# Performance work log

Hardware: AMD Instinct MI355X
Metric: run time of the kernel (lower is better)

Reference implementation:

```python
import jax, jax.numpy as jnp
import numpy as np

K = 9            # connections per output pixel
GA = 2           # global additional samples
RA = 2           # relative additional samples
VS = 4 + GA + RA # 2^rank neighbours + sampled
REGION = 12      # int(0.25 * 48) per spatial dim
MMULT = 0.1
MIN_SIGMA = 0.05
SIGMA_SCALE = 0.05
SIGMA_BOOST = 2.0


def setup_inputs() -> dict:
    key = jax.random.key(0)
    ks = jax.random.split(key, 8)
    b, cin, h, w = 8, 128, 48, 48
    cout = 256
    hidden = cin * 4

    def lin_init(k, fan_out, fan_in):
        bound = 1.0 / np.sqrt(fan_in)
        kw, kb = jax.random.split(k)
        W = jax.random.uniform(kw, (fan_out, fan_in), minval=-bound, maxval=bound, dtype=jnp.float32)
        bb = jax.random.uniform(kb, (fan_out,), minval=-bound, maxval=bound, dtype=jnp.float32)
        return W, bb

    x = jax.random.normal(ks[0], (b, cin, h, w), dtype=jnp.float32)
    W1, b1 = lin_init(ks[1], hidden, 2)          # toparams layer 1 (adaptive=False -> 2 coord inputs)
    W2, b2 = lin_init(ks[2], 3 * K, hidden)      # toparams layer 2 -> k means (2d) + k sigmas
    Wu, bu = lin_init(ks[3], cout, K * cin)      # unify linear
    gints = jax.random.randint(ks[4], (b, h, w, K, GA, 2), 0, h, dtype=jnp.int32)      # global samples (h==w)
    roff = jax.random.randint(ks[5], (b, h, w, K, RA, 2), 0, REGION, dtype=jnp.int32)  # relative offsets
    return {"x": x, "W1": W1, "b1": b1, "W2": W2, "b2": b2, "Wu": Wu, "bu": bu,
            "gints": gints, "roff": roff}


def reference(x, W1, b1, W2, b2, Wu, bu, gints, roff):
    b, c, h, w = x.shape
    s = jnp.array([h, w], dtype=x.dtype)                       # spatial range per dim
    s_int = jnp.array([h, w], dtype=jnp.int32)

    # normalized coordinate grid in [0,1], (h, w, 2) with [.,.,0]=row, [.,.,1]=col
    rows = jnp.arange(h, dtype=x.dtype) / (h - 1)
    cols = jnp.arange(w, dtype=x.dtype) / (w - 1)
    coords = jnp.stack(jnp.meshgrid(rows, cols, indexing='ij'), axis=-1)

    # hypernetwork: per-pixel coords -> K 2d mean offsets + K sigmas
    inp = jnp.broadcast_to(coords, (b, h, w, 2))
    hid = jax.nn.relu(inp @ W1.T + b1)
    params = hid @ W2.T + b2                                   # (b,h,w,3K)
    means_raw = params[..., :2 * K].reshape(b, h, w, K, 2)
    sig_raw = params[..., 2 * K:]                              # (b,h,w,K)

    # mids: inverse of the sigmoid scaling applied to the pixel's own coordinate
    pix = coords * (s - 1)                                     # pixel coordinates
    sc = pix / (s - 1) * 0.9999 + 0.00005
    mids = jnp.log(sc / (1.0 - sc))                            # (h,w,2)

    # transform_means: sigmoid -> [0, s-1]
    means = jax.nn.sigmoid(mids[None, :, :, None, :] + MMULT * means_raw) * (s - 1)  # (b,h,w,K,2)
    # transform_sigmas: softplus(. + boost) + min, per-dim scale, then sigma_scale
    sigmas = (jax.nn.softplus(sig_raw + SIGMA_BOOST) + MIN_SIGMA)[..., None] * s * SIGMA_SCALE  # (b,h,w,K,2)

    # ---- integer index generation (non-differentiable) ----
    fl = jnp.floor(jax.lax.stop_gradient(means)).astype(jnp.int32)   # (b,h,w,K,2)
    combos = jnp.array([[0, 0], [0, 1], [1, 0], [1, 1]], dtype=jnp.int32)
    neigh = fl[..., None, :] + combos                                 # (b,h,w,K,4,2)
    rel = fl[..., None, :] + roff - REGION // 2                       # (b,h,w,K,RA,2)
    ints = jnp.concatenate([neigh, gints, rel], axis=-2) % s_int      # (b,h,w,K,VS,2)

    # duplicate masking: zero any tuple that occurred earlier along VS
    eq = jnp.all(ints[..., :, None, :] == ints[..., None, :, :], axis=-1)  # (...,VS,VS)
    lower = jnp.tril(jnp.ones((VS, VS), dtype=bool), k=-1)
    dups = jnp.any(eq & lower, axis=-1)                               # (b,h,w,K,VS)

    # unnormalized gaussian densities of integer points under (means, sigmas)
    diff = (ints.astype(x.dtype) - means[..., None, :]) / sigmas[..., None, :]
    props = jnp.exp(-0.5 * jnp.sum(diff * diff, axis=-1))             # (b,h,w,K,VS)
    props = jnp.where(dups, jnp.zeros((), x.dtype), props)
    weights = props / jnp.sum(props, axis=-1, keepdims=True)          # mvalues are all-ones

    # irregular gather of input channel vectors at sampled pixels
    lin = ints[..., 0] * w + ints[..., 1]                             # (b,h,w,K,VS)
    flat = x.transpose(0, 2, 3, 1).reshape(b, h * w, c)
    feats = flat[jnp.arange(b)[:, None], lin.reshape(b, -1)]          # (b, h*w*K*VS, c)
    feats = feats.reshape(b, h, w, K, VS, c)

    feats = jnp.einsum('bhwkvc,bhwkv->bhwkc', feats, weights)         # weighted reduce over VS
    feats = feats.reshape(b, h, w, K * c)
    out = feats @ Wu.T + bu                                           # unify linear
    return out.transpose(0, 3, 1, 2)                                  # (b, cout, h, w)
```

## Files before the change

kernel.cpp:

```cpp
#include <hip/hip_runtime.h>
#include <hip/hip_bf16.h>
#include <hip/hip_fp16.h>

#define BB 8
#define CIN 128
#define HH 48
#define WW 48
#define HW 2304
#define KK 9
#define COUT 256
#define KC 1152
#define MM 18432
#define MT 16
#define SFP 136

#define LIGHT_BARRIER() asm volatile("s_waitcnt lgkmcnt(0)\n\ts_barrier" ::: "memory")

typedef short bf16x8_t __attribute__((ext_vector_type(8)));
typedef float f32x4_t  __attribute__((ext_vector_type(4)));

static __device__ __forceinline__ float b2f(short u) {
    union { unsigned int i; float f; } c;
    c.i = ((unsigned int)(unsigned short)u) << 16;
    return c.f;
}

__global__ __launch_bounds__(256) void prep_kernel(
    const float* __restrict__ x, __hip_bfloat16* __restrict__ xT,
    const float* __restrict__ Wu, bf16x8_t* __restrict__ Bp,
    const float* __restrict__ W1, const float* __restrict__ b1,
    const float* __restrict__ W2, const float* __restrict__ b2,
    float* __restrict__ means, float* __restrict__ sigmas, int* __restrict__ fls)
{
    __shared__ double s_par[4][27];
    int bid = blockIdx.x;
    int t = threadIdx.x;

    if (bid < 576) {
        __shared__ float tile[64][65];
        int ij0 = (bid % 36) * 64;
        int c0  = ((bid / 36) % 2) * 64;
        int b   = bid / 72;
        int ijl = t & 63, cl = t >> 6;
        #pragma unroll
        for (int i = 0; i < 16; i++) {
            int cc = i*4 + cl;
            tile[cc][ijl] = x[(size_t)(b*CIN + c0 + cc) * HW + ij0 + ijl];
        }
        __syncthreads();
        int cl2 = t & 63, ijl2 = t >> 6;
        #pragma unroll
        for (int i = 0; i < 16; i++) {
            int ij = i*4 + ijl2;
            xT[(size_t)(b*HW + ij0 + ij) * CIN + c0 + cl2] = __float2bfloat16(tile[cl2][ij]);
        }
    } else if (bid < 720) {
        int idx = (bid - 576) * 256 + t;
        int lane = idx & 63;
        int rest = idx >> 6;
        int ksub = rest % 36, tile16 = rest / 36;
        const float* src = Wu + (size_t)(tile16*16 + (lane & 15)) * KC
                              + ksub*32 + (lane >> 4)*8;
        union { bf16x8_t v; __hip_bfloat16 h[8]; } o;
        #pragma unroll
        for (int j = 0; j < 8; j++) o.h[j] = __float2bfloat16(src[j]);
        Bp[idx] = o.v;
    } else {
        int wave = t >> 6, lane = t & 63;
        int p = (bid - 720) * 4 + wave;
        int iy = p / WW, ix = p % WW;
        float ryf = (float)iy / 47.0f;
        float rxf = (float)ix / 47.0f;
        double ry = (double)ryf, rx = (double)rxf;

        double h[8];
        #pragma unroll
        for (int jj = 0; jj < 8; jj++) {
            int j = lane*8 + jj;
            double v = ry * (double)W1[j*2+0] + rx * (double)W1[j*2+1] + (double)b1[j];
            h[jj] = v > 0.0 ? v : 0.0;
        }
        for (int g = 0; g < 3; g++) {
            double par[9];
            #pragma unroll
            for (int oo = 0; oo < 9; oo++) {
                int o = g*9 + oo;
                const float4* w4 = (const float4*)(W2 + (size_t)o*512 + lane*8);
                float4 wa = w4[0], wb = w4[1];
                double s = (double)wa.x*h[0] + (double)wa.y*h[1]
                         + (double)wa.z*h[2] + (double)wa.w*h[3]
                         + (double)wb.x*h[4] + (double)wb.y*h[5]
                         + (double)wb.z*h[6] + (double)wb.w*h[7];
                par[oo] = s;
            }
            #pragma unroll
            for (int oo = 0; oo < 9; oo++) {
                #pragma unroll
                for (int d = 1; d < 64; d <<= 1)
                    par[oo] += __shfl_xor(par[oo], d, 64);
            }
            if (lane == 0) {
                #pragma unroll
                for (int oo = 0; oo < 9; oo++)
                    s_par[wave][g*9 + oo] = par[oo] + (double)b2[g*9 + oo];
            }
        }
        __syncthreads();
        if (lane < KK) {
            int k = lane;
            double scy = ry * 0.9999 + 5e-05;
            double scx = rx * 0.9999 + 5e-05;
            double midy = log(scy / (1.0 - scy));
            double midx = log(scx / (1.0 - scx));
            double zy = midy + 0.1 * s_par[wave][2*k+0];
            double zx = midx + 0.1 * s_par[wave][2*k+1];
            double my = 47.0 / (1.0 + exp(-zy));
            double mx = 47.0 / (1.0 + exp(-zx));
            double sr = s_par[wave][18 + k] + 2.0;
            double sp = (sr > 0.0 ? sr : 0.0) + log1p(exp(-fabs(sr)));
            double sg = (sp + 0.05) * 48.0 * 0.05;
            means[(p*KK + k)*2 + 0] = (float)my;
            means[(p*KK + k)*2 + 1] = (float)mx;
            sigmas[p*KK + k] = (float)sg;
            fls[(p*KK + k)*2 + 0] = (int)floor(my);
            fls[(p*KK + k)*2 + 1] = (int)floor(mx);
        }
    }
}

__global__ __launch_bounds__(256, 4) void fused_kernel(
    const float* __restrict__ means, const float* __restrict__ sigmas,
    const int* __restrict__ fls, const int* __restrict__ gints,
    const int* __restrict__ roff, const short* __restrict__ xT,
    const bf16x8_t* __restrict__ Bp, const float* __restrict__ bu,
    float* __restrict__ out)
{
    __shared__ unsigned int s_tap[KK*MT*8];
    __shared__ __align__(16) short s_feat[5][MT*SFP];

    int t = threadIdx.x;
    int b   = blockIdx.x & 7;
    int grp = blockIdx.x >> 3;
    int ij0 = grp * MT;
    int m0  = b * HW + ij0;

    if (t < KK*MT) {
        int p = t;
        int k = p >> 4, row = p & 15;
        int ij = ij0 + row;
        int bij = m0 + row;
        int fy = fls[(ij*KK + k)*2 + 0];
        int fx = fls[(ij*KK + k)*2 + 1];
        float my = means[(ij*KK + k)*2 + 0];
        float mx = means[(ij*KK + k)*2 + 1];
        float sg = sigmas[ij*KK + k];
        int lins[8]; float ws[8];
        #pragma unroll
        for (int v = 0; v < 8; v++) {
            int iy, ix;
            if (v < 4) {
                iy = fy + (v >> 1); ix = fx + (v & 1);
            } else if (v < 6) {
                int base = ((bij*KK + k)*2 + (v - 4)) * 2;
                iy = gints[base]; ix = gints[base + 1];
            } else {
                int base = ((bij*KK + k)*2 + (v - 6)) * 2;
                iy = fy + roff[base] - 6; ix = fx + roff[base + 1] - 6;
            }
            iy = ((iy % HH) + HH) % HH;
            ix = ((ix % WW) + WW) % WW;
            lins[v] = iy * WW + ix;
            float dy = ((float)iy - my) / sg;
            float dx = ((float)ix - mx) / sg;
            ws[v] = expf(-0.5f * (dy*dy + dx*dx));
        }
        #pragma unroll
        for (int v = 1; v < 8; v++) {
            bool dup = false;
            #pragma unroll
            for (int u = 0; u < 8; u++) if (u < v) dup = dup || (lins[u] == lins[v]);
            if (dup) ws[v] = 0.0f;
        }
        float sum = 0.0f;
        #pragma unroll
        for (int v = 0; v < 8; v++) sum += ws[v];
        float inv = 1.0f / sum;
        #pragma unroll
        for (int v = 0; v < 8; v++) {
            unsigned short hb = __half_as_ushort(__float2half(ws[v] * inv));
            s_tap[p*8+v] = ((unsigned int)lins[v] << 16) | (unsigned int)hb;
        }
    }
    LIGHT_BARRIER();

    const short* xb = xT + (size_t)b * (HW * CIN);
    int lane = t & 63, wave = t >> 6;
    int grow = t >> 4, gc0 = (t & 15) << 3;
    int arow = lane & 15, aq = lane >> 4;

    f32x4_t acc[4] = {};
    bf16x8_t tap[8];
    float    wgt[8];
    {
        const unsigned int* tp = &s_tap[(0*MT + grow)*8];
        #pragma unroll
        for (int v = 0; v < 8; v++) {
            unsigned int e = tp[v];
            wgt[v] = __half2float(__ushort_as_half((unsigned short)(e & 0xffffu)));
            tap[v] = *(const bf16x8_t*)(xb + (size_t)(e >> 16) * CIN + gc0);
        }
    }

    for (int k = 0; k < 5; k++) {
        float a0[8];
        #pragma unroll
        for (int j = 0; j < 8; j++) a0[j] = 0.0f;
        #pragma unroll
        for (int v = 0; v < 8; v++) {
            float w = wgt[v]; bf16x8_t d8 = tap[v];
            #pragma unroll
            for (int j = 0; j < 8; j++) a0[j] += w * b2f(d8[j]);
        }
        {
            const unsigned int* tp = &s_tap[((k+1)*MT + grow)*8];
            #pragma unroll
            for (int v = 0; v < 8; v++) {
                unsigned int e = tp[v];
                wgt[v] = __half2float(__ushort_as_half((unsigned short)(e & 0xffffu)));
                tap[v] = *(const bf16x8_t*)(xb + (size_t)(e >> 16) * CIN + gc0);
            }
        }
        union { bf16x8_t v8; __hip_bfloat16 hh[8]; } o;
        #pragma unroll
        for (int j = 0; j < 8; j++) o.hh[j] = __float2bfloat16(a0[j]);
        *(bf16x8_t*)(&s_feat[k][grow*SFP + gc0]) = o.v8;
    }
    LIGHT_BARRIER();
    for (int k = 0; k < 5; k++) {
        bf16x8_t Bf[16];
        {
            int base = (wave*4*36 + k*4)*64 + lane;
            #pragma unroll
            for (int tl = 0; tl < 4; tl++)
                #pragma unroll
                for (int s4 = 0; s4 < 4; s4++)
                    Bf[tl*4 + s4] = Bp[base + (tl*36 + s4)*64];
        }
        const short* fb = s_feat[k];
        bf16x8_t av[4];
        #pragma unroll
        for (int s4 = 0; s4 < 4; s4++)
            av[s4] = *(const bf16x8_t*)(fb + arow*SFP + s4*32 + aq*8);
        #pragma unroll
        for (int tl = 0; tl < 4; tl++)
            #pragma unroll
            for (int s4 = 0; s4 < 4; s4++)
                acc[tl] = __builtin_amdgcn_mfma_f32_16x16x32_bf16(av[s4], Bf[tl*4 + s4], acc[tl], 0, 0, 0);
    }
    LIGHT_BARRIER();
    for (int k = 5; k < KK; k++) {
        float a0[8];
        #pragma unroll
        for (int j = 0; j < 8; j++) a0[j] = 0.0f;
        #pragma unroll
        for (int v = 0; v < 8; v++) {
            float w = wgt[v]; bf16x8_t d8 = tap[v];
            #pragma unroll
            for (int j = 0; j < 8; j++) a0[j] += w * b2f(d8[j]);
        }
        if (k < KK - 1) {
            const unsigned int* tp = &s_tap[((k+1)*MT + grow)*8];
            #pragma unroll
            for (int v = 0; v < 8; v++) {
                unsigned int e = tp[v];
                wgt[v] = __half2float(__ushort_as_half((unsigned short)(e & 0xffffu)));
                tap[v] = *(const bf16x8_t*)(xb + (size_t)(e >> 16) * CIN + gc0);
            }
        }
        union { bf16x8_t v8; __hip_bfloat16 hh[8]; } o;
        #pragma unroll
        for (int j = 0; j < 8; j++) o.hh[j] = __float2bfloat16(a0[j]);
        *(bf16x8_t*)(&s_feat[k-5][grow*SFP + gc0]) = o.v8;
    }
    LIGHT_BARRIER();
    for (int k = 5; k < KK; k++) {
        bf16x8_t Bf[16];
        {
            int base = (wave*4*36 + k*4)*64 + lane;
            #pragma unroll
            for (int tl = 0; tl < 4; tl++)
                #pragma unroll
                for (int s4 = 0; s4 < 4; s4++)
                    Bf[tl*4 + s4] = Bp[base + (tl*36 + s4)*64];
        }
        const short* fb = s_feat[k-5];
        bf16x8_t av[4];
        #pragma unroll
        for (int s4 = 0; s4 < 4; s4++)
            av[s4] = *(const bf16x8_t*)(fb + arow*SFP + s4*32 + aq*8);
        #pragma unroll
        for (int tl = 0; tl < 4; tl++)
            #pragma unroll
            for (int s4 = 0; s4 < 4; s4++)
                acc[tl] = __builtin_amdgcn_mfma_f32_16x16x32_bf16(av[s4], Bf[tl*4 + s4], acc[tl], 0, 0, 0);
    }

    #pragma unroll
    for (int tl = 0; tl < 4; tl++) {
        int n = (wave*4 + tl)*16 + arow;
        float bv = bu[n];
        f32x4_t vv;
        vv[0] = acc[tl][0] + bv;
        vv[1] = acc[tl][1] + bv;
        vv[2] = acc[tl][2] + bv;
        vv[3] = acc[tl][3] + bv;
        *(f32x4_t*)(out + ((size_t)b * COUT + n) * HW + ij0 + aq*4) = vv;
    }
}

extern "C" void kernel_launch(void* const* d_in, const int* in_sizes, int n_in,
                              void* d_out, int out_size, void* d_ws, size_t ws_size,
                              hipStream_t stream)
{
    const float* x   = (const float*)d_in[0];
    const float* W1  = (const float*)d_in[1];
    const float* b1  = (const float*)d_in[2];
    const float* W2  = (const float*)d_in[3];
    const float* b2  = (const float*)d_in[4];
    const float* Wu  = (const float*)d_in[5];
    const float* bu  = (const float*)d_in[6];
    const int* gints = (const int*)d_in[7];
    const int* roff  = (const int*)d_in[8];
    float* out = (float*)d_out;

    char* ws = (char*)d_ws;
    float* ws_means  = (float*)(ws + 0);
    float* ws_sigma  = (float*)(ws + 165888);
    int*   ws_fl     = (int*  )(ws + 248832);
    short* ws_xT     = (short*)(ws + 414720);
    bf16x8_t* ws_bp  = (bf16x8_t*)(ws + 5133312);

    prep_kernel<<<1296, 256, 0, stream>>>(x, (__hip_bfloat16*)ws_xT, Wu, ws_bp,
                                          W1, b1, W2, b2,
                                          ws_means, ws_sigma, ws_fl);
    fused_kernel<<<MM/MT, 256, 0, stream>>>(ws_means, ws_sigma, ws_fl, gints, roff,
                                            ws_xT, ws_bp, bu, out);
}
```

Before: 144.9 us.

## Split tap weight computation into separate kernel using all threads

Measured after the change: 150.1 us. 3.5% more time.

```diff
diff --git a/kernel.cpp b/kernel.cpp
--- a/kernel.cpp
+++ b/kernel.cpp
@@ -128,14 +128,64 @@
     }
 }
 
-__global__ __launch_bounds__(256, 4) void fused_kernel(
+__global__ __launch_bounds__(256) void taps_kernel(
     const float* __restrict__ means, const float* __restrict__ sigmas,
     const int* __restrict__ fls, const int* __restrict__ gints,
-    const int* __restrict__ roff, const short* __restrict__ xT,
+    const int* __restrict__ roff, unsigned int* __restrict__ tapout)
+{
+    int e = blockIdx.x * 256 + threadIdx.x;
+    int bij = e / KK, k = e - bij*KK;
+    int ij = bij % HW;
+
+    int fy = fls[(ij*KK + k)*2 + 0];
+    int fx = fls[(ij*KK + k)*2 + 1];
+    float my = means[(ij*KK + k)*2 + 0];
+    float mx = means[(ij*KK + k)*2 + 1];
+    float sg = sigmas[ij*KK + k];
+    int lins[8]; float ws[8];
+    #pragma unroll
+    for (int v = 0; v < 8; v++) {
+        int iy, ix;
+        if (v < 4) {
+            iy = fy + (v >> 1); ix = fx + (v & 1);
+        } else if (v < 6) {
+            int base = ((bij*KK + k)*2 + (v - 4)) * 2;
+            iy = gints[base]; ix = gints[base + 1];
+        } else {
+            int base = ((bij*KK + k)*2 + (v - 6)) * 2;
+            iy = fy + roff[base] - 6; ix = fx + roff[base + 1] - 6;
+        }
+        iy = ((iy % HH) + HH) % HH;
+        ix = ((ix % WW) + WW) % WW;
+        lins[v] = iy * WW + ix;
+        float dy = ((float)iy - my) / sg;
+        float dx = ((float)ix - mx) / sg;
+        ws[v] = expf(-0.5f * (dy*dy + dx*dx));
+    }
+    #pragma unroll
+    for (int v = 1; v < 8; v++) {
+        bool dup = false;
+        #pragma unroll
+        for (int u = 0; u < 8; u++) if (u < v) dup = dup || (lins[u] == lins[v]);
+        if (dup) ws[v] = 0.0f;
+    }
+    float sum = 0.0f;
+    #pragma unroll
+    for (int v = 0; v < 8; v++) sum += ws[v];
+    float inv = 1.0f / sum;
+    #pragma unroll
+    for (int v = 0; v < 8; v++) {
+        unsigned short hb = __half_as_ushort(__float2half(ws[v] * inv));
+        tapout[(size_t)e*8 + v] = ((unsigned int)lins[v] << 16) | (unsigned int)hb;
+    }
+}
+
+__global__ __launch_bounds__(256, 4) void fused_kernel(
+    const unsigned int* __restrict__ tapg, const short* __restrict__ xT,
     const bf16x8_t* __restrict__ Bp, const float* __restrict__ bu,
     float* __restrict__ out)
 {
-    __shared__ unsigned int s_tap[KK*MT*8];
+    __shared__ unsigned int s_tap[MT*KK*8];
     __shared__ __align__(16) short s_feat[5][MT*SFP];
 
     int t = threadIdx.x;
@@ -144,51 +194,12 @@
     int ij0 = grp * MT;
     int m0  = b * HW + ij0;
 
-    if (t < KK*MT) {
-        int p = t;
-        int k = p >> 4, row = p & 15;
-        int ij = ij0 + row;
-        int bij = m0 + row;
-        int fy = fls[(ij*KK + k)*2 + 0];
-        int fx = fls[(ij*KK + k)*2 + 1];
-        float my = means[(ij*KK + k)*2 + 0];
-        float mx = means[(ij*KK + k)*2 + 1];
-        float sg = sigmas[ij*KK + k];
-        int lins[8]; float ws[8];
-        #pragma unroll
-        for (int v = 0; v < 8; v++) {
-            int iy, ix;
-            if (v < 4) {
-                iy = fy + (v >> 1); ix = fx + (v & 1);
-            } else if (v < 6) {
-                int base = ((bij*KK + k)*2 + (v - 4)) * 2;
-                iy = gints[base]; ix = gints[base + 1];
-            } else {
-                int base = ((bij*KK + k)*2 + (v - 6)) * 2;
-                iy = fy + roff[base] - 6; ix = fx + roff[base + 1] - 6;
-            }
-            iy = ((iy % HH) + HH) % HH;
-            ix = ((ix % WW) + WW) % WW;
-            lins[v] = iy * WW + ix;
-            float dy = ((float)iy - my) / sg;
-            float dx = ((float)ix - mx) / sg;
-            ws[v] = expf(-0.5f * (dy*dy + dx*dx));
-        }
-        #pragma unroll
-        for (int v = 1; v < 8; v++) {
-            bool dup = false;
-            #pragma unroll
-            for (int u = 0; u < 8; u++) if (u < v) dup = dup || (lins[u] == lins[v]);
-            if (dup) ws[v] = 0.0f;
-        }
-        float sum = 0.0f;
-        #pragma unroll
-        for (int v = 0; v < 8; v++) sum += ws[v];
-        float inv = 1.0f / sum;
-        #pragma unroll
-        for (int v = 0; v < 8; v++) {
-            unsigned short hb = __half_as_ushort(__float2half(ws[v] * inv));
-            s_tap[p*8+v] = ((unsigned int)lins[v] << 16) | (unsigned int)hb;
+    {
+        const unsigned int* tg = tapg + (size_t)m0 * (KK*8);
+        #pragma unroll
+        for (int i = 0; i < (MT*KK*8)/256 + 1; i++) {
+            int idx = i*256 + t;
+            if (idx < MT*KK*8) s_tap[idx] = tg[idx];
         }
     }
     LIGHT_BARRIER();
@@ -202,7 +213,7 @@
     bf16x8_t tap[8];
     float    wgt[8];
     {
-        const unsigned int* tp = &s_tap[(0*MT + grow)*8];
+        const unsigned int* tp = &s_tap[(grow*KK + 0)*8];
         #pragma unroll
         for (int v = 0; v < 8; v++) {
             unsigned int e = tp[v];
@@ -222,7 +233,7 @@
             for (int j = 0; j < 8; j++) a0[j] += w * b2f(d8[j]);
         }
         {
-            const unsigned int* tp = &s_tap[((k+1)*MT + grow)*8];
+            const unsigned int* tp = &s_tap[(grow*KK + k+1)*8];
             #pragma unroll
             for (int v = 0; v < 8; v++) {
                 unsigned int e = tp[v];
@@ -269,7 +280,7 @@
             for (int j = 0; j < 8; j++) a0[j] += w * b2f(d8[j]);
         }
         if (k < KK - 1) {
-            const unsigned int* tp = &s_tap[((k+1)*MT + grow)*8];
+            const unsigned int* tp = &s_tap[(grow*KK + k+1)*8];
             #pragma unroll
             for (int v = 0; v < 8; v++) {
                 unsigned int e = tp[v];
@@ -339,10 +350,12 @@
     int*   ws_fl     = (int*  )(ws + 248832);
     short* ws_xT     = (short*)(ws + 414720);
     bf16x8_t* ws_bp  = (bf16x8_t*)(ws + 5133312);
+    unsigned int* ws_tap = (unsigned int*)(ws + 5723136);
 
     prep_kernel<<<1296, 256, 0, stream>>>(x, (__hip_bfloat16*)ws_xT, Wu, ws_bp,
                                           W1, b1, W2, b2,
                                           ws_means, ws_sigma, ws_fl);
-    fused_kernel<<<MM/MT, 256, 0, stream>>>(ws_means, ws_sigma, ws_fl, gints, roff,
-                                            ws_xT, ws_bp, bu, out);
-}
+    taps_kernel<<<648, 256, 0, stream>>>(ws_means, ws_sigma, ws_fl, gints, roff,
+                                         ws_tap);
+    fused_kernel<<<MM/MT, 256, 0, stream>>>(ws_tap, ws_xT, ws_bp, bu, out);
+}
```
